# Kernel tuning notes

Measured on AMD Instinct MI355X. Metric: run time of the kernel, lower is better.

## Reference

```python
import jax, jax.numpy as jnp
import numpy as np

HIDDEN = 256
HEADS = 8
HEAD_DIM = HIDDEN // HEADS
SCALE = HEAD_DIM ** -0.5
N = 4096
NUM_GRAPHS = 16
LN_EPS = 1e-5


def setup_inputs() -> dict:
    key = jax.random.key(0)
    ks = jax.random.split(key, 8)
    x = jax.random.normal(ks[0], (N, HIDDEN), dtype=jnp.float32)
    batch = jnp.sort(jax.random.randint(ks[1], (N,), 0, NUM_GRAPHS, dtype=jnp.int64))
    # Xavier-uniform linear weights, stored as [in, out] (y = x @ W + b)
    lim = float(np.sqrt(6.0 / (HIDDEN + HIDDEN)))
    def W(k):
        return jax.random.uniform(k, (HIDDEN, HIDDEN), jnp.float32, -lim, lim)
    return {
        "x": x,
        "batch": batch,
        "Wq": W(ks[2]), "bq": jnp.zeros((HIDDEN,), jnp.float32),
        "Wk": W(ks[3]), "bk": jnp.zeros((HIDDEN,), jnp.float32),
        "Wv": W(ks[4]), "bv": jnp.zeros((HIDDEN,), jnp.float32),
        "Wo": W(ks[5]), "bo": jnp.zeros((HIDDEN,), jnp.float32),
        "gamma": jnp.ones((HIDDEN,), jnp.float32),
        "beta": jnp.zeros((HIDDEN,), jnp.float32),
    }


def _layer_norm(x, gamma, beta):
    mu = jnp.mean(x, axis=-1, keepdims=True)
    var = jnp.mean(jnp.square(x - mu), axis=-1, keepdims=True)
    return (x - mu) * jax.lax.rsqrt(var + LN_EPS) * gamma + beta


def reference(x, batch, Wq, bq, Wk, bk, Wv, bv, Wo, bo, gamma, beta):
    residual = x
    h = _layer_norm(x, gamma, beta)
    n = h.shape[0]
    q = (h @ Wq + bq).reshape(n, HEADS, HEAD_DIM)
    k = (h @ Wk + bk).reshape(n, HEADS, HEAD_DIM)
    v = (h @ Wv + bv).reshape(n, HEADS, HEAD_DIM)
    # dense scores masked to block-diagonal (same-graph) structure
    scores = jnp.einsum('ihd,jhd->ihj', q, k) * SCALE  # [N, H, N]
    same_graph = (batch[None, :] == batch[:, None])[:, None, :]  # [N, 1, N]
    scores = jnp.where(same_graph, scores, -jnp.inf)
    attn = jax.nn.softmax(scores, axis=-1)
    attn = jnp.nan_to_num(attn, nan=0.0)
    out = jnp.einsum('ihj,jhd->ihd', attn, v).reshape(n, HIDDEN)
    out = out @ Wo + bo
    return residual + out
```

## Files before the change

kernel.cpp:

```cpp
#include <hip/hip_runtime.h>

#define NNODES 4096
#define HID 256
#define NG 16
#define NH 8
#define HD 32
#define LN_EPS 1e-5f
#define QSCALE (0.17677669529663687f * 1.4426950408889634f)
#define CAPT 384
#define KLS 40
#define VTS (CAPT + 2)

typedef unsigned short u16;
typedef unsigned int u32;
typedef __bf16 bf16x8 __attribute__((ext_vector_type(8)));
typedef float f32x4 __attribute__((ext_vector_type(4)));

__device__ __forceinline__ float bf2f(u16 u){
  union { u32 i; float f; } c; c.i = ((u32)u) << 16; return c.f;
}
__device__ __forceinline__ u16 f2bf(float f){
  union { float f; u32 i; } c; c.f = f;
  u32 x = c.i;
  return (u16)((x + 0x7fffu + ((x >> 16) & 1u)) >> 16);
}

__global__ __launch_bounds__(256) void prep_kernel(
    const float* __restrict__ x, const float* __restrict__ gamma,
    const float* __restrict__ beta, u16* __restrict__ h,
    const float* __restrict__ Wq, const float* __restrict__ Wk,
    const float* __restrict__ Wv, const float* __restrict__ Wo,
    u16* __restrict__ Wt, const int* __restrict__ bw, int* __restrict__ seg){
  __shared__ u16 tile[32][33];
  __shared__ int bad;
  int b = blockIdx.x;
  if (b < 1024){
    int wave = threadIdx.x >> 6, lane = threadIdx.x & 63;
    int row = b * 4 + wave;
    float4 xv = ((const float4*)x)[row * 64 + lane];
    float a0 = xv.x, a1 = xv.y, a2 = xv.z, a3 = xv.w;
    float s = a0 + a1 + a2 + a3;
    #pragma unroll
    for (int m = 1; m < 64; m <<= 1) s += __shfl_xor(s, m);
    float mu = s * (1.0f / HID);
    float d0 = a0 - mu, d1 = a1 - mu, d2 = a2 - mu, d3 = a3 - mu;
    float vv = d0*d0 + d1*d1 + d2*d2 + d3*d3;
    #pragma unroll
    for (int m = 1; m < 64; m <<= 1) vv += __shfl_xor(vv, m);
    float rs = rsqrtf(vv * (1.0f / HID) + LN_EPS);
    float4 gv = ((const float4*)gamma)[lane];
    float4 bv = ((const float4*)beta)[lane];
    ushort4 o;
    o.x = f2bf(d0 * rs * gv.x + bv.x);
    o.y = f2bf(d1 * rs * gv.y + bv.y);
    o.z = f2bf(d2 * rs * gv.z + bv.z);
    o.w = f2bf(d3 * rs * gv.w + bv.w);
    *(ushort4*)(h + (size_t)row * HID + lane * 4) = o;
  } else if (b < 1280){
    int idx = b - 1024;
    int w = idx >> 6;
    int t = idx & 63;
    int bx = (t & 7) * 32, by = (t >> 3) * 32;
    const float* src = (w == 0) ? Wq : (w == 1) ? Wk : (w == 2) ? Wv : Wo;
    u16* dst = Wt + (size_t)w * HID * HID;
    int tx = threadIdx.x & 31, ty = threadIdx.x >> 5;
    #pragma unroll
    for (int r = 0; r < 32; r += 8)
      tile[ty + r][tx] = f2bf(src[(size_t)(by + ty + r) * HID + bx + tx]);
    __syncthreads();
    #pragma unroll
    for (int r = 0; r < 32; r += 8)
      dst[(size_t)(bx + ty + r) * HID + by + tx] = tile[tx][ty + r];
  } else {
    if (threadIdx.x == 0) bad = 0;
    __syncthreads();
    int local_bad = 0;
    for (int i = threadIdx.x; i < NNODES; i += 256){
      int v = bw[i];
      if (v < 0 || v > 15) local_bad = 1;
      if (i + 1 < NNODES && bw[i + 1] < v) local_bad = 1;
    }
    if (local_bad) atomicOr(&bad, 1);
    __syncthreads();
    int stride = bad ? 2 : 1;
    int g = threadIdx.x;
    if (g <= NG){
      int lo = 0, hi = NNODES;
      while (lo < hi){
        int mid = (lo + hi) >> 1;
        if (bw[mid * stride] < g) lo = mid + 1; else hi = mid;
      }
      seg[g] = lo;
    }
  }
}

template<bool FINAL>
__device__ __forceinline__ void gemm_tile(const u16* __restrict__ A, const u16* __restrict__ Bt,
    const float* __restrict__ bias, const float* __restrict__ resid, void* __restrict__ out){
  int gw = blockIdx.x * 4 + (threadIdx.x >> 6);
  int lane = threadIdx.x & 63;
  int lr = lane & 15, lq = lane >> 4;
  int m0 = (gw >> 4) * 64;
  int n0 = (gw & 15) * 16;
  f32x4 acc[4] = {};
  const u16* arow = A + (size_t)(m0 + lr) * HID + lq * 8;
  const u16* brow = Bt + (size_t)(n0 + lr) * HID + lq * 8;
  #pragma unroll
  for (int k0 = 0; k0 < HID; k0 += 32){
    bf16x8 b = *(const bf16x8*)(brow + k0);
    #pragma unroll
    for (int t = 0; t < 4; t++){
      bf16x8 a = *(const bf16x8*)(arow + (size_t)t * 16 * HID + k0);
      acc[t] = __builtin_amdgcn_mfma_f32_16x16x32_bf16(a, b, acc[t], 0, 0, 0);
    }
  }
  int col = n0 + lr;
  float bb = bias[col];
  #pragma unroll
  for (int t = 0; t < 4; t++){
    #pragma unroll
    for (int r = 0; r < 4; r++){
      int row = m0 + 16 * t + lq * 4 + r;
      float val = acc[t][r] + bb;
      if (FINAL){
        val += resid[(size_t)row * HID + col];
        ((float*)out)[(size_t)row * HID + col] = val;
      } else {
        ((u16*)out)[(size_t)row * HID + col] = f2bf(val);
      }
    }
  }
}

__global__ __launch_bounds__(256) void gemm_qkv_kernel(const u16* __restrict__ h,
    const u16* __restrict__ Wt, const float* __restrict__ bq, const float* __restrict__ bk,
    const float* __restrict__ bv, u16* __restrict__ q, u16* __restrict__ k, u16* __restrict__ v){
  int which = blockIdx.y;
  const u16* B = Wt + (size_t)which * HID * HID;
  const float* bias = (which == 0) ? bq : (which == 1) ? bk : bv;
  u16* out = (which == 0) ? q : (which == 1) ? k : v;
  gemm_tile<false>(h, B, bias, nullptr, out);
}

__global__ __launch_bounds__(256) void gemm_proj_kernel(const u16* __restrict__ ao,
    const u16* __restrict__ WtO, const float* __restrict__ bo, const float* __restrict__ x,
    float* __restrict__ out){
  gemm_tile<true>(ao, WtO, bo, x, out);
}

__global__ __launch_bounds__(512, 4) void attn_kernel(const u16* __restrict__ q,
    const u16* __restrict__ k, const u16* __restrict__ v, const int* __restrict__ seg,
    u16* __restrict__ out){
  __shared__ u16 kl[CAPT * KLS];
  __shared__ u16 vt[HD * VTS];
  __shared__ float mg[4][10][64];
  int gh = blockIdx.y;
  int g = gh >> 3, hd = gh & 7;
  int start = seg[g], end = seg[g + 1];
  int len = end - start;
  if (len <= 0) return;
  if (len > CAPT) len = CAPT;
  int ntj = (len + 15) >> 4;
  int nj16 = ntj << 4;
  for (int idx = threadIdx.x; idx < nj16 * 4; idx += 512){
    int row = idx >> 2, part = idx & 3;
    uint4 val = make_uint4(0, 0, 0, 0);
    if (row < len)
      val = *(const uint4*)&k[(size_t)(start + row) * HID + hd * HD + part * 8];
    *(uint4*)&kl[row * KLS + part * 8] = val;
  }
  for (int idx = threadIdx.x; idx < nj16 * 4; idx += 512){
    int row = idx >> 2, part = idx & 3;
    uint4 w = make_uint4(0, 0, 0, 0);
    if (row < len)
      w = *(const uint4*)&v[(size_t)(start + row) * HID + hd * HD + part * 8];
    int d0 = part * 8;
    vt[(d0 + 0) * VTS + row] = (u16)(w.x & 0xffffu);
    vt[(d0 + 1) * VTS + row] = (u16)(w.x >> 16);
    vt[(d0 + 2) * VTS + row] = (u16)(w.y & 0xffffu);
    vt[(d0 + 3) * VTS + row] = (u16)(w.y >> 16);
    vt[(d0 + 4) * VTS + row] = (u16)(w.z & 0xffffu);
    vt[(d0 + 5) * VTS + row] = (u16)(w.z >> 16);
    vt[(d0 + 6) * VTS + row] = (u16)(w.w & 0xffffu);
    vt[(d0 + 7) * VTS + row] = (u16)(w.w >> 16);
  }
  __syncthreads();
  int wave = threadIdx.x >> 6, lane = threadIdx.x & 63;
  int lq = lane >> 4, lr = lane & 15;
  int tl = wave & 3;
  int jh = wave >> 2;
  int nouter = (ntj + 15) >> 4;
  for (int it = 0; it < nouter; it++){
    int tq = it * 16 + blockIdx.x * 4 + tl;
    bool active = tq < ntj;
    int q0 = tq << 4;
    float m = -3.0e38f, l = 0.f;
    f32x4 o0 = {0.f,0.f,0.f,0.f}, o1 = {0.f,0.f,0.f,0.f};
    if (active){
      bf16x8 qf = *(const bf16x8*)&q[(size_t)(start + q0 + lr) * HID + hd * HD + lq * 8];
      int half = (ntj + 1) >> 1;
      int jt0 = jh ? half : 0;
      int jt1 = jh ? ntj : half;
      for (int jt = jt0; jt < jt1; jt++){
        int j0 = jt << 4;
        bf16x8 kf = *(const bf16x8*)&kl[(j0 + lr) * KLS + lq * 8];
        f32x4 st = __builtin_amdgcn_mfma_f32_16x16x32_bf16(kf, qf,
                     (f32x4){0.f,0.f,0.f,0.f}, 0, 0, 0);
        int jb = j0 + lq * 4;
        float s0 = (jb + 0 < len) ? st[0] * QSCALE : -3.0e38f;
        float s1 = (jb + 1 < len) ? st[1] * QSCALE : -3.0e38f;
        float s2 = (jb + 2 < len) ? st[2] * QSCALE : -3.0e38f;
        float s3 = (jb + 3 < len) ? st[3] * QSCALE : -3.0e38f;
        float tm = fmaxf(fmaxf(s0, s1), fmaxf(s2, s3));
        tm = fmaxf(tm, __shfl_xor(tm, 16));
        tm = fmaxf(tm, __shfl_xor(tm, 32));
        float mn = fmaxf(m, tm);
        float alpha = exp2f(m - mn);
        float p0 = exp2f(s0 - mn), p1 = exp2f(s1 - mn);
        float p2 = exp2f(s2 - mn), p3 = exp2f(s3 - mn);
        float ps = (p0 + p1) + (p2 + p3);
        ps += __shfl_xor(ps, 16);
        ps += __shfl_xor(ps, 32);
        l = l * alpha + ps;
        m = mn;
        union { bf16x8 v8; u32 w[4]; } pf, vf0, vf1;
        pf.w[0] = (u32)f2bf(p0) | ((u32)f2bf(p1) << 16);
        pf.w[1] = (u32)f2bf(p2) | ((u32)f2bf(p3) << 16);
        pf.w[2] = 0; pf.w[3] = 0;
        const u16* vp0 = &vt[lr * VTS + j0 + lq * 4];
        const u16* vp1 = &vt[(16 + lr) * VTS + j0 + lq * 4];
        vf0.w[0] = *(const u32*)vp0; vf0.w[1] = *(const u32*)(vp0 + 2);
        vf0.w[2] = 0; vf0.w[3] = 0;
        vf1.w[0] = *(const u32*)vp1; vf1.w[1] = *(const u32*)(vp1 + 2);
        vf1.w[2] = 0; vf1.w[3] = 0;
        o0 = o0 * alpha;
        o1 = o1 * alpha;
        o0 = __builtin_amdgcn_mfma_f32_16x16x32_bf16(vf0.v8, pf.v8, o0, 0, 0, 0);
        o1 = __builtin_amdgcn_mfma_f32_16x16x32_bf16(vf1.v8, pf.v8, o1, 0, 0, 0);
      }
    }
    if (jh == 1){
      mg[tl][0][lane] = o0[0]; mg[tl][1][lane] = o0[1];
      mg[tl][2][lane] = o0[2]; mg[tl][3][lane] = o0[3];
      mg[tl][4][lane] = o1[0]; mg[tl][5][lane] = o1[1];
      mg[tl][6][lane] = o1[2]; mg[tl][7][lane] = o1[3];
      mg[tl][8][lane] = m;     mg[tl][9][lane] = l;
    }
    __syncthreads();
    if (jh == 0 && active && q0 + lr < len){
      float m2 = mg[tl][8][lane], l2 = mg[tl][9][lane];
      float mn = fmaxf(m, m2);
      float a  = exp2f(m - mn);
      float a2 = exp2f(m2 - mn);
      float lt = l * a + l2 * a2;
      float rl = 1.0f / lt;
      float r0 = (o0[0]*a + mg[tl][0][lane]*a2) * rl;
      float r1 = (o0[1]*a + mg[tl][1][lane]*a2) * rl;
      float r2 = (o0[2]*a + mg[tl][2][lane]*a2) * rl;
      float r3 = (o0[3]*a + mg[tl][3][lane]*a2) * rl;
      float r4 = (o1[0]*a + mg[tl][4][lane]*a2) * rl;
      float r5 = (o1[1]*a + mg[tl][5][lane]*a2) * rl;
      float r6 = (o1[2]*a + mg[tl][6][lane]*a2) * rl;
      float r7 = (o1[3]*a + mg[tl][7][lane]*a2) * rl;
      u16* orow = out + (size_t)(start + q0 + lr) * HID + hd * HD;
      int dbase = lq * 4;
      *(u32*)&orow[dbase]          = (u32)f2bf(r0) | ((u32)f2bf(r1) << 16);
      *(u32*)&orow[dbase + 2]      = (u32)f2bf(r2) | ((u32)f2bf(r3) << 16);
      *(u32*)&orow[16 + dbase]     = (u32)f2bf(r4) | ((u32)f2bf(r5) << 16);
      *(u32*)&orow[16 + dbase + 2] = (u32)f2bf(r6) | ((u32)f2bf(r7) << 16);
    }
    __syncthreads();
  }
}

__global__ void sentinel_kernel(u32* __restrict__ out, int nwords){
  int i = blockIdx.x * 256 + threadIdx.x;
  if (i < nwords) out[i] = 0x46404640u;
}

extern "C" void kernel_launch(void* const* d_in, const int* in_sizes, int n_in,
                              void* d_out, int out_size, void* d_ws, size_t ws_size,
                              hipStream_t stream){
  const float* x   = (const float*)d_in[0];
  const int* batch = (const int*)d_in[1];
  const float* Wq = (const float*)d_in[2],  *bq = (const float*)d_in[3];
  const float* Wk = (const float*)d_in[4],  *bk = (const float*)d_in[5];
  const float* Wv = (const float*)d_in[6],  *bv = (const float*)d_in[7];
  const float* Wo = (const float*)d_in[8],  *bo = (const float*)d_in[9];
  const float* gamma = (const float*)d_in[10], *beta = (const float*)d_in[11];

  const size_t WT_OFF  = 1024;
  const size_t QKV_OFF = WT_OFF + 4 * HID * HID * 2;
  const size_t BUF     = (size_t)NNODES * HID * 2;
  const size_t NEED    = QKV_OFF + 4 * BUF;

  if (ws_size < NEED){
    int nwords = out_size / 2;
    sentinel_kernel<<<(nwords + 255) / 256, 256, 0, stream>>>((u32*)d_out, nwords);
    return;
  }

  char* w = (char*)d_ws;
  int* seg  = (int*)(w + 128);
  u16* Wt   = (u16*)(w + WT_OFF);
  u16* qb   = (u16*)(w + QKV_OFF);
  u16* kb   = qb + (size_t)NNODES * HID;
  u16* vb   = kb + (size_t)NNODES * HID;
  u16* ao   = vb + (size_t)NNODES * HID;
  u16* h    = (u16*)d_out;

  prep_kernel<<<1281, 256, 0, stream>>>(x, gamma, beta, h, Wq, Wk, Wv, Wo, Wt, batch, seg);
  gemm_qkv_kernel<<<dim3(256, 3), 256, 0, stream>>>(h, Wt, bq, bk, bv, qb, kb, vb);
  attn_kernel<<<dim3(4, NG * NH), 512, 0, stream>>>(qb, kb, vb, seg, ao);
  gemm_proj_kernel<<<256, 256, 0, stream>>>(ao, Wt + 3 * (size_t)HID * HID, bo, x, (float*)d_out);
}
```

Measured before the change: 128.7 us.

## Fuse QKV projection into attention kernel per graph-head block

Removes the separate QKV GEMM kernel and computes K and V for the whole graph segment and Q for the block's query tiles directly inside the attention kernel, writing them to shared memory instead of global buffers. Each of the two blocks per (graph, head) redundantly recomputes the full K/V projection for its segment. The split-key two-wave merge with its extra shared buffer and barriers is dropped: each wave now processes all key tiles for its query tile. This saves a kernel launch and the global round-trip for q/k/v. In exchange it duplicates K/V compute across blocks and reads weights straight from global/L2 without tiling reuse.

```diff
diff --git a/kernel.cpp b/kernel.cpp
--- a/kernel.cpp
+++ b/kernel.cpp
@@ -10,6 +10,7 @@
 #define CAPT 384
 #define KLS 40
 #define VTS (CAPT + 2)
+#define QSL 12
 
 typedef unsigned short u16;
 typedef unsigned int u32;
@@ -133,144 +134,144 @@
   }
 }
 
-__global__ __launch_bounds__(256) void gemm_qkv_kernel(const u16* __restrict__ h,
-    const u16* __restrict__ Wt, const float* __restrict__ bq, const float* __restrict__ bk,
-    const float* __restrict__ bv, u16* __restrict__ q, u16* __restrict__ k, u16* __restrict__ v){
-  int which = blockIdx.y;
-  const u16* B = Wt + (size_t)which * HID * HID;
-  const float* bias = (which == 0) ? bq : (which == 1) ? bk : bv;
-  u16* out = (which == 0) ? q : (which == 1) ? k : v;
-  gemm_tile<false>(h, B, bias, nullptr, out);
-}
-
 __global__ __launch_bounds__(256) void gemm_proj_kernel(const u16* __restrict__ ao,
     const u16* __restrict__ WtO, const float* __restrict__ bo, const float* __restrict__ x,
     float* __restrict__ out){
   gemm_tile<true>(ao, WtO, bo, x, out);
 }
 
-__global__ __launch_bounds__(512, 4) void attn_kernel(const u16* __restrict__ q,
-    const u16* __restrict__ k, const u16* __restrict__ v, const int* __restrict__ seg,
+__global__ __launch_bounds__(512, 4) void qkv_attn_kernel(
+    const u16* __restrict__ h, const u16* __restrict__ Wt,
+    const float* __restrict__ bq, const float* __restrict__ bk,
+    const float* __restrict__ bv, const int* __restrict__ seg,
     u16* __restrict__ out){
   __shared__ u16 kl[CAPT * KLS];
   __shared__ u16 vt[HD * VTS];
-  __shared__ float mg[4][10][64];
+  __shared__ u16 ql[QSL * 16 * KLS];
   int gh = blockIdx.y;
   int g = gh >> 3, hd = gh & 7;
+  int bid = blockIdx.x;
   int start = seg[g], end = seg[g + 1];
   int len = end - start;
   if (len <= 0) return;
   if (len > CAPT) len = CAPT;
   int ntj = (len + 15) >> 4;
-  int nj16 = ntj << 4;
-  for (int idx = threadIdx.x; idx < nj16 * 4; idx += 512){
-    int row = idx >> 2, part = idx & 3;
-    uint4 val = make_uint4(0, 0, 0, 0);
-    if (row < len)
-      val = *(const uint4*)&k[(size_t)(start + row) * HID + hd * HD + part * 8];
-    *(uint4*)&kl[row * KLS + part * 8] = val;
-  }
-  for (int idx = threadIdx.x; idx < nj16 * 4; idx += 512){
-    int row = idx >> 2, part = idx & 3;
-    uint4 w = make_uint4(0, 0, 0, 0);
-    if (row < len)
-      w = *(const uint4*)&v[(size_t)(start + row) * HID + hd * HD + part * 8];
-    int d0 = part * 8;
-    vt[(d0 + 0) * VTS + row] = (u16)(w.x & 0xffffu);
-    vt[(d0 + 1) * VTS + row] = (u16)(w.x >> 16);
-    vt[(d0 + 2) * VTS + row] = (u16)(w.y & 0xffffu);
-    vt[(d0 + 3) * VTS + row] = (u16)(w.y >> 16);
-    vt[(d0 + 4) * VTS + row] = (u16)(w.z & 0xffffu);
-    vt[(d0 + 5) * VTS + row] = (u16)(w.z >> 16);
-    vt[(d0 + 6) * VTS + row] = (u16)(w.w & 0xffffu);
-    vt[(d0 + 7) * VTS + row] = (u16)(w.w >> 16);
-  }
-  __syncthreads();
   int wave = threadIdx.x >> 6, lane = threadIdx.x & 63;
   int lq = lane >> 4, lr = lane & 15;
-  int tl = wave & 3;
-  int jh = wave >> 2;
-  int nouter = (ntj + 15) >> 4;
-  for (int it = 0; it < nouter; it++){
-    int tq = it * 16 + blockIdx.x * 4 + tl;
-    bool active = tq < ntj;
-    int q0 = tq << 4;
+
+  const u16* wq0p = Wt + (size_t)(hd * HD + lr) * HID;
+  const u16* wk0p = wq0p + (size_t)HID * HID;
+  const u16* wv0p = wq0p + (size_t)2 * HID * HID;
+  float bq0 = bq[hd * HD + lr],      bq1 = bq[hd * HD + 16 + lr];
+  float bk0 = bk[hd * HD + lr],      bk1 = bk[hd * HD + 16 + lr];
+  float bv0 = bv[hd * HD + lr],      bv1 = bv[hd * HD + 16 + lr];
+
+  for (int t = wave; t < ntj; t += 8){
+    f32x4 ak0 = {}, ak1 = {}, av0 = {}, av1 = {};
+    int row = start + (t << 4) + lr;
+    if (row >= NNODES) row = NNODES - 1;
+    const u16* hrow = h + (size_t)row * HID + lq * 8;
+    #pragma unroll 2
+    for (int k0 = 0; k0 < HID; k0 += 32){
+      bf16x8 a    = *(const bf16x8*)(hrow + k0);
+      bf16x8 wk0f = *(const bf16x8*)(wk0p + k0 + lq * 8);
+      bf16x8 wk1f = *(const bf16x8*)(wk0p + 16 * HID + k0 + lq * 8);
+      bf16x8 wv0f = *(const bf16x8*)(wv0p + k0 + lq * 8);
+      bf16x8 wv1f = *(const bf16x8*)(wv0p + 16 * HID + k0 + lq * 8);
+      ak0 = __builtin_amdgcn_mfma_f32_16x16x32_bf16(a, wk0f, ak0, 0, 0, 0);
+      ak1 = __builtin_amdgcn_mfma_f32_16x16x32_bf16(a, wk1f, ak1, 0, 0, 0);
+      av0 = __builtin_amdgcn_mfma_f32_16x16x32_bf16(a, wv0f, av0, 0, 0, 0);
+      av1 = __builtin_amdgcn_mfma_f32_16x16x32_bf16(a, wv1f, av1, 0, 0, 0);
+    }
+    int jr = (t << 4) + lq * 4;
+    #pragma unroll
+    for (int r = 0; r < 4; r++){
+      kl[(jr + r) * KLS + lr]      = f2bf(ak0[r] + bk0);
+      kl[(jr + r) * KLS + 16 + lr] = f2bf(ak1[r] + bk1);
+    }
+    *(u32*)&vt[lr * VTS + jr]            = (u32)f2bf(av0[0] + bv0) | ((u32)f2bf(av0[1] + bv0) << 16);
+    *(u32*)&vt[lr * VTS + jr + 2]        = (u32)f2bf(av0[2] + bv0) | ((u32)f2bf(av0[3] + bv0) << 16);
+    *(u32*)&vt[(16 + lr) * VTS + jr]     = (u32)f2bf(av1[0] + bv1) | ((u32)f2bf(av1[1] + bv1) << 16);
+    *(u32*)&vt[(16 + lr) * VTS + jr + 2] = (u32)f2bf(av1[2] + bv1) | ((u32)f2bf(av1[3] + bv1) << 16);
+  }
+
+  for (int s = wave; s < QSL; s += 8){
+    int t = (s << 1) + bid;
+    if (t >= ntj) continue;
+    f32x4 aq0 = {}, aq1 = {};
+    int row = start + (t << 4) + lr;
+    if (row >= NNODES) row = NNODES - 1;
+    const u16* hrow = h + (size_t)row * HID + lq * 8;
+    #pragma unroll 2
+    for (int k0 = 0; k0 < HID; k0 += 32){
+      bf16x8 a    = *(const bf16x8*)(hrow + k0);
+      bf16x8 wq0f = *(const bf16x8*)(wq0p + k0 + lq * 8);
+      bf16x8 wq1f = *(const bf16x8*)(wq0p + 16 * HID + k0 + lq * 8);
+      aq0 = __builtin_amdgcn_mfma_f32_16x16x32_bf16(a, wq0f, aq0, 0, 0, 0);
+      aq1 = __builtin_amdgcn_mfma_f32_16x16x32_bf16(a, wq1f, aq1, 0, 0, 0);
+    }
+    int qr = (s << 4) + lq * 4;
+    #pragma unroll
+    for (int r = 0; r < 4; r++){
+      ql[(qr + r) * KLS + lr]      = f2bf(aq0[r] + bq0);
+      ql[(qr + r) * KLS + 16 + lr] = f2bf(aq1[r] + bq1);
+    }
+  }
+  __syncthreads();
+
+  for (int s = wave; s < QSL; s += 8){
+    int t = (s << 1) + bid;
+    if (t >= ntj) continue;
+    int q0 = t << 4;
+    bf16x8 qf = *(const bf16x8*)&ql[((s << 4) + lr) * KLS + lq * 8];
     float m = -3.0e38f, l = 0.f;
     f32x4 o0 = {0.f,0.f,0.f,0.f}, o1 = {0.f,0.f,0.f,0.f};
-    if (active){
-      bf16x8 qf = *(const bf16x8*)&q[(size_t)(start + q0 + lr) * HID + hd * HD + lq * 8];
-      int half = (ntj + 1) >> 1;
-      int jt0 = jh ? half : 0;
-      int jt1 = jh ? ntj : half;
-      for (int jt = jt0; jt < jt1; jt++){
-        int j0 = jt << 4;
-        bf16x8 kf = *(const bf16x8*)&kl[(j0 + lr) * KLS + lq * 8];
-        f32x4 st = __builtin_amdgcn_mfma_f32_16x16x32_bf16(kf, qf,
-                     (f32x4){0.f,0.f,0.f,0.f}, 0, 0, 0);
-        int jb = j0 + lq * 4;
-        float s0 = (jb + 0 < len) ? st[0] * QSCALE : -3.0e38f;
-        float s1 = (jb + 1 < len) ? st[1] * QSCALE : -3.0e38f;
-        float s2 = (jb + 2 < len) ? st[2] * QSCALE : -3.0e38f;
-        float s3 = (jb + 3 < len) ? st[3] * QSCALE : -3.0e38f;
-        float tm = fmaxf(fmaxf(s0, s1), fmaxf(s2, s3));
-        tm = fmaxf(tm, __shfl_xor(tm, 16));
-        tm = fmaxf(tm, __shfl_xor(tm, 32));
-        float mn = fmaxf(m, tm);
-        float alpha = exp2f(m - mn);
-        float p0 = exp2f(s0 - mn), p1 = exp2f(s1 - mn);
-        float p2 = exp2f(s2 - mn), p3 = exp2f(s3 - mn);
-        float ps = (p0 + p1) + (p2 + p3);
-        ps += __shfl_xor(ps, 16);
-        ps += __shfl_xor(ps, 32);
-        l = l * alpha + ps;
-        m = mn;
-        union { bf16x8 v8; u32 w[4]; } pf, vf0, vf1;
-        pf.w[0] = (u32)f2bf(p0) | ((u32)f2bf(p1) << 16);
-        pf.w[1] = (u32)f2bf(p2) | ((u32)f2bf(p3) << 16);
-        pf.w[2] = 0; pf.w[3] = 0;
-        const u16* vp0 = &vt[lr * VTS + j0 + lq * 4];
-        const u16* vp1 = &vt[(16 + lr) * VTS + j0 + lq * 4];
-        vf0.w[0] = *(const u32*)vp0; vf0.w[1] = *(const u32*)(vp0 + 2);
-        vf0.w[2] = 0; vf0.w[3] = 0;
-        vf1.w[0] = *(const u32*)vp1; vf1.w[1] = *(const u32*)(vp1 + 2);
-        vf1.w[2] = 0; vf1.w[3] = 0;
-        o0 = o0 * alpha;
-        o1 = o1 * alpha;
-        o0 = __builtin_amdgcn_mfma_f32_16x16x32_bf16(vf0.v8, pf.v8, o0, 0, 0, 0);
-        o1 = __builtin_amdgcn_mfma_f32_16x16x32_bf16(vf1.v8, pf.v8, o1, 0, 0, 0);
-      }
-    }
-    if (jh == 1){
-      mg[tl][0][lane] = o0[0]; mg[tl][1][lane] = o0[1];
-      mg[tl][2][lane] = o0[2]; mg[tl][3][lane] = o0[3];
-      mg[tl][4][lane] = o1[0]; mg[tl][5][lane] = o1[1];
-      mg[tl][6][lane] = o1[2]; mg[tl][7][lane] = o1[3];
-      mg[tl][8][lane] = m;     mg[tl][9][lane] = l;
-    }
-    __syncthreads();
-    if (jh == 0 && active && q0 + lr < len){
-      float m2 = mg[tl][8][lane], l2 = mg[tl][9][lane];
-      float mn = fmaxf(m, m2);
-      float a  = exp2f(m - mn);
-      float a2 = exp2f(m2 - mn);
-      float lt = l * a + l2 * a2;
-      float rl = 1.0f / lt;
-      float r0 = (o0[0]*a + mg[tl][0][lane]*a2) * rl;
-      float r1 = (o0[1]*a + mg[tl][1][lane]*a2) * rl;
-      float r2 = (o0[2]*a + mg[tl][2][lane]*a2) * rl;
-      float r3 = (o0[3]*a + mg[tl][3][lane]*a2) * rl;
-      float r4 = (o1[0]*a + mg[tl][4][lane]*a2) * rl;
-      float r5 = (o1[1]*a + mg[tl][5][lane]*a2) * rl;
-      float r6 = (o1[2]*a + mg[tl][6][lane]*a2) * rl;
-      float r7 = (o1[3]*a + mg[tl][7][lane]*a2) * rl;
+    for (int jt = 0; jt < ntj; jt++){
+      int j0 = jt << 4;
+      bf16x8 kf = *(const bf16x8*)&kl[(j0 + lr) * KLS + lq * 8];
+      f32x4 st = __builtin_amdgcn_mfma_f32_16x16x32_bf16(kf, qf,
+                   (f32x4){0.f,0.f,0.f,0.f}, 0, 0, 0);
+      int jb = j0 + lq * 4;
+      float s0 = (jb + 0 < len) ? st[0] * QSCALE : -3.0e38f;
+      float s1 = (jb + 1 < len) ? st[1] * QSCALE : -3.0e38f;
+      float s2 = (jb + 2 < len) ? st[2] * QSCALE : -3.0e38f;
+      float s3 = (jb + 3 < len) ? st[3] * QSCALE : -3.0e38f;
+      float tm = fmaxf(fmaxf(s0, s1), fmaxf(s2, s3));
+      tm = fmaxf(tm, __shfl_xor(tm, 16));
+      tm = fmaxf(tm, __shfl_xor(tm, 32));
+      float mn = fmaxf(m, tm);
+      float alpha = exp2f(m - mn);
+      float p0 = exp2f(s0 - mn), p1 = exp2f(s1 - mn);
+      float p2 = exp2f(s2 - mn), p3 = exp2f(s3 - mn);
+      float ps = (p0 + p1) + (p2 + p3);
+      ps += __shfl_xor(ps, 16);
+      ps += __shfl_xor(ps, 32);
+      l = l * alpha + ps;
+      m = mn;
+      union { bf16x8 v8; u32 w[4]; } pf, vf0, vf1;
+      pf.w[0] = (u32)f2bf(p0) | ((u32)f2bf(p1) << 16);
+      pf.w[1] = (u32)f2bf(p2) | ((u32)f2bf(p3) << 16);
+      pf.w[2] = 0; pf.w[3] = 0;
+      const u16* vp0 = &vt[lr * VTS + j0 + lq * 4];
+      const u16* vp1 = &vt[(16 + lr) * VTS + j0 + lq * 4];
+      vf0.w[0] = *(const u32*)vp0; vf0.w[1] = *(const u32*)(vp0 + 2);
+      vf0.w[2] = 0; vf0.w[3] = 0;
+      vf1.w[0] = *(const u32*)vp1; vf1.w[1] = *(const u32*)(vp1 + 2);
+      vf1.w[2] = 0; vf1.w[3] = 0;
+      o0 = o0 * alpha;
+      o1 = o1 * alpha;
+      o0 = __builtin_amdgcn_mfma_f32_16x16x32_bf16(vf0.v8, pf.v8, o0, 0, 0, 0);
+      o1 = __builtin_amdgcn_mfma_f32_16x16x32_bf16(vf1.v8, pf.v8, o1, 0, 0, 0);
+    }
+    if (q0 + lr < len){
+      float rl = 1.0f / l;
       u16* orow = out + (size_t)(start + q0 + lr) * HID + hd * HD;
       int dbase = lq * 4;
-      *(u32*)&orow[dbase]          = (u32)f2bf(r0) | ((u32)f2bf(r1) << 16);
-      *(u32*)&orow[dbase + 2]      = (u32)f2bf(r2) | ((u32)f2bf(r3) << 16);
-      *(u32*)&orow[16 + dbase]     = (u32)f2bf(r4) | ((u32)f2bf(r5) << 16);
-      *(u32*)&orow[16 + dbase + 2] = (u32)f2bf(r6) | ((u32)f2bf(r7) << 16);
-    }
-    __syncthreads();
+      *(u32*)&orow[dbase]          = (u32)f2bf(o0[0]*rl) | ((u32)f2bf(o0[1]*rl) << 16);
+      *(u32*)&orow[dbase + 2]      = (u32)f2bf(o0[2]*rl) | ((u32)f2bf(o0[3]*rl) << 16);
+      *(u32*)&orow[16 + dbase]     = (u32)f2bf(o1[0]*rl) | ((u32)f2bf(o1[1]*rl) << 16);
+      *(u32*)&orow[16 + dbase + 2] = (u32)f2bf(o1[2]*rl) | ((u32)f2bf(o1[3]*rl) << 16);
+    }
   }
 }
 
@@ -290,10 +291,10 @@
   const float* Wo = (const float*)d_in[8],  *bo = (const float*)d_in[9];
   const float* gamma = (const float*)d_in[10], *beta = (const float*)d_in[11];
 
-  const size_t WT_OFF  = 1024;
-  const size_t QKV_OFF = WT_OFF + 4 * HID * HID * 2;
-  const size_t BUF     = (size_t)NNODES * HID * 2;
-  const size_t NEED    = QKV_OFF + 4 * BUF;
+  const size_t WT_OFF = 1024;
+  const size_t AO_OFF = WT_OFF + 4 * HID * HID * 2;
+  const size_t BUF    = (size_t)NNODES * HID * 2;
+  const size_t NEED   = AO_OFF + BUF;
 
   if (ws_size < NEED){
     int nwords = out_size / 2;
@@ -304,14 +305,10 @@
   char* w = (char*)d_ws;
   int* seg  = (int*)(w + 128);
   u16* Wt   = (u16*)(w + WT_OFF);
-  u16* qb   = (u16*)(w + QKV_OFF);
-  u16* kb   = qb + (size_t)NNODES * HID;
-  u16* vb   = kb + (size_t)NNODES * HID;
-  u16* ao   = vb + (size_t)NNODES * HID;
+  u16* ao   = (u16*)(w + AO_OFF);
   u16* h    = (u16*)d_out;
 
   prep_kernel<<<1281, 256, 0, stream>>>(x, gamma, beta, h, Wq, Wk, Wv, Wo, Wt, batch, seg);
-  gemm_qkv_kernel<<<dim3(256, 3), 256, 0, stream>>>(h, Wt, bq, bk, bv, qb, kb, vb);
-  attn_kernel<<<dim3(4, NG * NH), 512, 0, stream>>>(qb, kb, vb, seg, ao);
+  qkv_attn_kernel<<<dim3(2, NG * NH), 512, 0, stream>>>(h, Wt, bq, bk, bv, seg, ao);
   gemm_proj_kernel<<<256, 256, 0, stream>>>(ao, Wt + 3 * (size_t)HID * HID, bo, x, (float*)d_out);
 }
```

Result: slower. 136.0 us (+5.7%).

## Fuse all stages into one cooperative persistent kernel with grid syncs

Applied to the files above, without the earlier changes.

Replaces the four separate launches (prep, QKV GEMM, attention, output projection) with a single cooperative kernel of 512 blocks that runs each phase in turn, separated by grid-wide barriers. It falls back to four ordinary launches if the cooperative launch fails. The QKV GEMM now computes Q, K and V together in each wave so the A tile is loaded once. Attention drops the split of key tiles across two wave halves and the shared-memory merge, so each wave processes all key tiles for its query tile. The aim is to remove launch gaps and tail effects between kernels, at the cost of grid-sync overhead, fewer blocks resident per stage, and less parallelism inside attention.

```diff
diff --git a/kernel.cpp b/kernel.cpp
--- a/kernel.cpp
+++ b/kernel.cpp
@@ -1,4 +1,7 @@
 #include <hip/hip_runtime.h>
+#include <hip/hip_cooperative_groups.h>
+
+namespace cg = cooperative_groups;
 
 #define NNODES 4096
 #define HID 256
@@ -16,28 +19,33 @@
 typedef __bf16 bf16x8 __attribute__((ext_vector_type(8)));
 typedef float f32x4 __attribute__((ext_vector_type(4)));
 
-__device__ __forceinline__ float bf2f(u16 u){
-  union { u32 i; float f; } c; c.i = ((u32)u) << 16; return c.f;
-}
 __device__ __forceinline__ u16 f2bf(float f){
   union { float f; u32 i; } c; c.f = f;
   u32 x = c.i;
   return (u16)((x + 0x7fffu + ((x >> 16) & 1u)) >> 16);
 }
 
-__global__ __launch_bounds__(256) void prep_kernel(
-    const float* __restrict__ x, const float* __restrict__ gamma,
-    const float* __restrict__ beta, u16* __restrict__ h,
-    const float* __restrict__ Wq, const float* __restrict__ Wk,
-    const float* __restrict__ Wv, const float* __restrict__ Wo,
-    u16* __restrict__ Wt, const int* __restrict__ bw, int* __restrict__ seg){
+struct Params {
+  const float* x; const int* batch;
+  const float* Wq; const float* bq;
+  const float* Wk; const float* bk;
+  const float* Wv; const float* bv;
+  const float* Wo; const float* bo;
+  const float* gamma; const float* beta;
+  int* seg; u16* Wt; u16* h; u16* qb; u16* kb; u16* vb; u16* ao;
+  float* out;
+};
+
+__device__ __forceinline__ void phaseA(const Params& p){
   __shared__ u16 tile[32][33];
   __shared__ int bad;
-  int b = blockIdx.x;
-  if (b < 1024){
-    int wave = threadIdx.x >> 6, lane = threadIdx.x & 63;
-    int row = b * 4 + wave;
-    float4 xv = ((const float4*)x)[row * 64 + lane];
+  int bid = blockIdx.x, tid = threadIdx.x;
+  int wave = tid >> 6, lane = tid & 63;
+  int wgid = bid * 4 + wave;
+  #pragma unroll
+  for (int ps = 0; ps < 2; ps++){
+    int row = wgid + ps * 2048;
+    float4 xv = ((const float4*)p.x)[row * 64 + lane];
     float a0 = xv.x, a1 = xv.y, a2 = xv.z, a3 = xv.w;
     float s = a0 + a1 + a2 + a3;
     #pragma unroll
@@ -48,22 +56,22 @@
     #pragma unroll
     for (int m = 1; m < 64; m <<= 1) vv += __shfl_xor(vv, m);
     float rs = rsqrtf(vv * (1.0f / HID) + LN_EPS);
-    float4 gv = ((const float4*)gamma)[lane];
-    float4 bv = ((const float4*)beta)[lane];
+    float4 gv = ((const float4*)p.gamma)[lane];
+    float4 bv = ((const float4*)p.beta)[lane];
     ushort4 o;
     o.x = f2bf(d0 * rs * gv.x + bv.x);
     o.y = f2bf(d1 * rs * gv.y + bv.y);
     o.z = f2bf(d2 * rs * gv.z + bv.z);
     o.w = f2bf(d3 * rs * gv.w + bv.w);
-    *(ushort4*)(h + (size_t)row * HID + lane * 4) = o;
-  } else if (b < 1280){
-    int idx = b - 1024;
-    int w = idx >> 6;
-    int t = idx & 63;
+    *(ushort4*)(p.h + (size_t)row * HID + lane * 4) = o;
+  }
+  if (bid < 256){
+    int w = bid >> 6;
+    int t = bid & 63;
     int bx = (t & 7) * 32, by = (t >> 3) * 32;
-    const float* src = (w == 0) ? Wq : (w == 1) ? Wk : (w == 2) ? Wv : Wo;
-    u16* dst = Wt + (size_t)w * HID * HID;
-    int tx = threadIdx.x & 31, ty = threadIdx.x >> 5;
+    const float* src = (w == 0) ? p.Wq : (w == 1) ? p.Wk : (w == 2) ? p.Wv : p.Wo;
+    u16* dst = p.Wt + (size_t)w * HID * HID;
+    int tx = tid & 31, ty = tid >> 5;
     #pragma unroll
     for (int r = 0; r < 32; r += 8)
       tile[ty + r][tx] = f2bf(src[(size_t)(by + ty + r) * HID + bx + tx]);
@@ -71,11 +79,13 @@
     #pragma unroll
     for (int r = 0; r < 32; r += 8)
       dst[(size_t)(bx + ty + r) * HID + by + tx] = tile[tx][ty + r];
-  } else {
-    if (threadIdx.x == 0) bad = 0;
+  }
+  if (bid == 511){
+    const int* bw = p.batch;
+    if (tid == 0) bad = 0;
     __syncthreads();
     int local_bad = 0;
-    for (int i = threadIdx.x; i < NNODES; i += 256){
+    for (int i = tid; i < NNODES; i += 256){
       int v = bw[i];
       if (v < 0 || v > 15) local_bad = 1;
       if (i + 1 < NNODES && bw[i + 1] < v) local_bad = 1;
@@ -83,98 +93,82 @@
     if (local_bad) atomicOr(&bad, 1);
     __syncthreads();
     int stride = bad ? 2 : 1;
-    int g = threadIdx.x;
+    int g = tid;
     if (g <= NG){
       int lo = 0, hi = NNODES;
       while (lo < hi){
         int mid = (lo + hi) >> 1;
         if (bw[mid * stride] < g) lo = mid + 1; else hi = mid;
       }
-      seg[g] = lo;
-    }
-  }
-}
-
-template<bool FINAL>
-__device__ __forceinline__ void gemm_tile(const u16* __restrict__ A, const u16* __restrict__ Bt,
-    const float* __restrict__ bias, const float* __restrict__ resid, void* __restrict__ out){
-  int gw = blockIdx.x * 4 + (threadIdx.x >> 6);
+      p.seg[g] = lo;
+    }
+  }
+}
+
+__device__ __forceinline__ void phaseB(const Params& p){
+  int wgid = blockIdx.x * 4 + (threadIdx.x >> 6);
   int lane = threadIdx.x & 63;
   int lr = lane & 15, lq = lane >> 4;
-  int m0 = (gw >> 4) * 64;
-  int n0 = (gw & 15) * 16;
-  f32x4 acc[4] = {};
-  const u16* arow = A + (size_t)(m0 + lr) * HID + lq * 8;
-  const u16* brow = Bt + (size_t)(n0 + lr) * HID + lq * 8;
+  int m0 = (wgid >> 4) * 32, n0 = (wgid & 15) * 16;
+  const u16* a0p = p.h + (size_t)(m0 + lr) * HID + lq * 8;
+  const u16* a1p = a0p + (size_t)16 * HID;
+  const u16* bqp = p.Wt + (size_t)(n0 + lr) * HID + lq * 8;
+  const u16* bkp = bqp + (size_t)HID * HID;
+  const u16* bvp = bqp + (size_t)2 * HID * HID;
+  f32x4 aq[2] = {}, ak[2] = {}, av[2] = {};
   #pragma unroll
   for (int k0 = 0; k0 < HID; k0 += 32){
-    bf16x8 b = *(const bf16x8*)(brow + k0);
-    #pragma unroll
-    for (int t = 0; t < 4; t++){
-      bf16x8 a = *(const bf16x8*)(arow + (size_t)t * 16 * HID + k0);
-      acc[t] = __builtin_amdgcn_mfma_f32_16x16x32_bf16(a, b, acc[t], 0, 0, 0);
-    }
+    bf16x8 a0 = *(const bf16x8*)(a0p + k0);
+    bf16x8 a1 = *(const bf16x8*)(a1p + k0);
+    bf16x8 wq = *(const bf16x8*)(bqp + k0);
+    bf16x8 wk = *(const bf16x8*)(bkp + k0);
+    bf16x8 wv = *(const bf16x8*)(bvp + k0);
+    aq[0] = __builtin_amdgcn_mfma_f32_16x16x32_bf16(a0, wq, aq[0], 0, 0, 0);
+    aq[1] = __builtin_amdgcn_mfma_f32_16x16x32_bf16(a1, wq, aq[1], 0, 0, 0);
+    ak[0] = __builtin_amdgcn_mfma_f32_16x16x32_bf16(a0, wk, ak[0], 0, 0, 0);
+    ak[1] = __builtin_amdgcn_mfma_f32_16x16x32_bf16(a1, wk, ak[1], 0, 0, 0);
+    av[0] = __builtin_amdgcn_mfma_f32_16x16x32_bf16(a0, wv, av[0], 0, 0, 0);
+    av[1] = __builtin_amdgcn_mfma_f32_16x16x32_bf16(a1, wv, av[1], 0, 0, 0);
   }
   int col = n0 + lr;
-  float bb = bias[col];
-  #pragma unroll
-  for (int t = 0; t < 4; t++){
+  float cq = p.bq[col], ck = p.bk[col], cv = p.bv[col];
+  #pragma unroll
+  for (int t = 0; t < 2; t++){
     #pragma unroll
     for (int r = 0; r < 4; r++){
-      int row = m0 + 16 * t + lq * 4 + r;
-      float val = acc[t][r] + bb;
-      if (FINAL){
-        val += resid[(size_t)row * HID + col];
-        ((float*)out)[(size_t)row * HID + col] = val;
-      } else {
-        ((u16*)out)[(size_t)row * HID + col] = f2bf(val);
-      }
-    }
-  }
-}
-
-__global__ __launch_bounds__(256) void gemm_qkv_kernel(const u16* __restrict__ h,
-    const u16* __restrict__ Wt, const float* __restrict__ bq, const float* __restrict__ bk,
-    const float* __restrict__ bv, u16* __restrict__ q, u16* __restrict__ k, u16* __restrict__ v){
-  int which = blockIdx.y;
-  const u16* B = Wt + (size_t)which * HID * HID;
-  const float* bias = (which == 0) ? bq : (which == 1) ? bk : bv;
-  u16* out = (which == 0) ? q : (which == 1) ? k : v;
-  gemm_tile<false>(h, B, bias, nullptr, out);
-}
-
-__global__ __launch_bounds__(256) void gemm_proj_kernel(const u16* __restrict__ ao,
-    const u16* __restrict__ WtO, const float* __restrict__ bo, const float* __restrict__ x,
-    float* __restrict__ out){
-  gemm_tile<true>(ao, WtO, bo, x, out);
-}
-
-__global__ __launch_bounds__(512, 4) void attn_kernel(const u16* __restrict__ q,
-    const u16* __restrict__ k, const u16* __restrict__ v, const int* __restrict__ seg,
-    u16* __restrict__ out){
+      size_t row = (size_t)(m0 + 16 * t + lq * 4 + r) * HID + col;
+      p.qb[row] = f2bf(aq[t][r] + cq);
+      p.kb[row] = f2bf(ak[t][r] + ck);
+      p.vb[row] = f2bf(av[t][r] + cv);
+    }
+  }
+}
+
+__device__ __forceinline__ void phaseC(const Params& p){
   __shared__ u16 kl[CAPT * KLS];
   __shared__ u16 vt[HD * VTS];
-  __shared__ float mg[4][10][64];
-  int gh = blockIdx.y;
+  int job = blockIdx.x;
+  int quarter = job & 3, gh = job >> 2;
   int g = gh >> 3, hd = gh & 7;
-  int start = seg[g], end = seg[g + 1];
+  int start = p.seg[g], end = p.seg[g + 1];
   int len = end - start;
   if (len <= 0) return;
   if (len > CAPT) len = CAPT;
   int ntj = (len + 15) >> 4;
   int nj16 = ntj << 4;
-  for (int idx = threadIdx.x; idx < nj16 * 4; idx += 512){
+  int tid = threadIdx.x;
+  for (int idx = tid; idx < nj16 * 4; idx += 256){
     int row = idx >> 2, part = idx & 3;
     uint4 val = make_uint4(0, 0, 0, 0);
     if (row < len)
-      val = *(const uint4*)&k[(size_t)(start + row) * HID + hd * HD + part * 8];
+      val = *(const uint4*)&p.kb[(size_t)(start + row) * HID + hd * HD + part * 8];
     *(uint4*)&kl[row * KLS + part * 8] = val;
   }
-  for (int idx = threadIdx.x; idx < nj16 * 4; idx += 512){
+  for (int idx = tid; idx < nj16 * 4; idx += 256){
     int row = idx >> 2, part = idx & 3;
     uint4 w = make_uint4(0, 0, 0, 0);
     if (row < len)
-      w = *(const uint4*)&v[(size_t)(start + row) * HID + hd * HD + part * 8];
+      w = *(const uint4*)&p.vb[(size_t)(start + row) * HID + hd * HD + part * 8];
     int d0 = part * 8;
     vt[(d0 + 0) * VTS + row] = (u16)(w.x & 0xffffu);
     vt[(d0 + 1) * VTS + row] = (u16)(w.x >> 16);
@@ -186,93 +180,111 @@
     vt[(d0 + 7) * VTS + row] = (u16)(w.w >> 16);
   }
   __syncthreads();
-  int wave = threadIdx.x >> 6, lane = threadIdx.x & 63;
+  int wave = tid >> 6, lane = tid & 63;
   int lq = lane >> 4, lr = lane & 15;
-  int tl = wave & 3;
-  int jh = wave >> 2;
   int nouter = (ntj + 15) >> 4;
   for (int it = 0; it < nouter; it++){
-    int tq = it * 16 + blockIdx.x * 4 + tl;
-    bool active = tq < ntj;
+    int tq = it * 16 + quarter * 4 + wave;
+    if (tq >= ntj) continue;
     int q0 = tq << 4;
+    bf16x8 qf = *(const bf16x8*)&p.qb[(size_t)(start + q0 + lr) * HID + hd * HD + lq * 8];
     float m = -3.0e38f, l = 0.f;
     f32x4 o0 = {0.f,0.f,0.f,0.f}, o1 = {0.f,0.f,0.f,0.f};
-    if (active){
-      bf16x8 qf = *(const bf16x8*)&q[(size_t)(start + q0 + lr) * HID + hd * HD + lq * 8];
-      int half = (ntj + 1) >> 1;
-      int jt0 = jh ? half : 0;
-      int jt1 = jh ? ntj : half;
-      for (int jt = jt0; jt < jt1; jt++){
-        int j0 = jt << 4;
-        bf16x8 kf = *(const bf16x8*)&kl[(j0 + lr) * KLS + lq * 8];
-        f32x4 st = __builtin_amdgcn_mfma_f32_16x16x32_bf16(kf, qf,
-                     (f32x4){0.f,0.f,0.f,0.f}, 0, 0, 0);
-        int jb = j0 + lq * 4;
-        float s0 = (jb + 0 < len) ? st[0] * QSCALE : -3.0e38f;
-        float s1 = (jb + 1 < len) ? st[1] * QSCALE : -3.0e38f;
-        float s2 = (jb + 2 < len) ? st[2] * QSCALE : -3.0e38f;
-        float s3 = (jb + 3 < len) ? st[3] * QSCALE : -3.0e38f;
-        float tm = fmaxf(fmaxf(s0, s1), fmaxf(s2, s3));
-        tm = fmaxf(tm, __shfl_xor(tm, 16));
-        tm = fmaxf(tm, __shfl_xor(tm, 32));
-        float mn = fmaxf(m, tm);
-        float alpha = exp2f(m - mn);
-        float p0 = exp2f(s0 - mn), p1 = exp2f(s1 - mn);
-        float p2 = exp2f(s2 - mn), p3 = exp2f(s3 - mn);
-        float ps = (p0 + p1) + (p2 + p3);
-        ps += __shfl_xor(ps, 16);
-        ps += __shfl_xor(ps, 32);
-        l = l * alpha + ps;
-        m = mn;
-        union { bf16x8 v8; u32 w[4]; } pf, vf0, vf1;
-        pf.w[0] = (u32)f2bf(p0) | ((u32)f2bf(p1) << 16);
-        pf.w[1] = (u32)f2bf(p2) | ((u32)f2bf(p3) << 16);
-        pf.w[2] = 0; pf.w[3] = 0;
-        const u16* vp0 = &vt[lr * VTS + j0 + lq * 4];
-        const u16* vp1 = &vt[(16 + lr) * VTS + j0 + lq * 4];
-        vf0.w[0] = *(const u32*)vp0; vf0.w[1] = *(const u32*)(vp0 + 2);
-        vf0.w[2] = 0; vf0.w[3] = 0;
-        vf1.w[0] = *(const u32*)vp1; vf1.w[1] = *(const u32*)(vp1 + 2);
-        vf1.w[2] = 0; vf1.w[3] = 0;
-        o0 = o0 * alpha;
-        o1 = o1 * alpha;
-        o0 = __builtin_amdgcn_mfma_f32_16x16x32_bf16(vf0.v8, pf.v8, o0, 0, 0, 0);
-        o1 = __builtin_amdgcn_mfma_f32_16x16x32_bf16(vf1.v8, pf.v8, o1, 0, 0, 0);
-      }
-    }
-    if (jh == 1){
-      mg[tl][0][lane] = o0[0]; mg[tl][1][lane] = o0[1];
-      mg[tl][2][lane] = o0[2]; mg[tl][3][lane] = o0[3];
-      mg[tl][4][lane] = o1[0]; mg[tl][5][lane] = o1[1];
-      mg[tl][6][lane] = o1[2]; mg[tl][7][lane] = o1[3];
-      mg[tl][8][lane] = m;     mg[tl][9][lane] = l;
-    }
-    __syncthreads();
-    if (jh == 0 && active && q0 + lr < len){
-      float m2 = mg[tl][8][lane], l2 = mg[tl][9][lane];
-      float mn = fmaxf(m, m2);
-      float a  = exp2f(m - mn);
-      float a2 = exp2f(m2 - mn);
-      float lt = l * a + l2 * a2;
-      float rl = 1.0f / lt;
-      float r0 = (o0[0]*a + mg[tl][0][lane]*a2) * rl;
-      float r1 = (o0[1]*a + mg[tl][1][lane]*a2) * rl;
-      float r2 = (o0[2]*a + mg[tl][2][lane]*a2) * rl;
-      float r3 = (o0[3]*a + mg[tl][3][lane]*a2) * rl;
-      float r4 = (o1[0]*a + mg[tl][4][lane]*a2) * rl;
-      float r5 = (o1[1]*a + mg[tl][5][lane]*a2) * rl;
-      float r6 = (o1[2]*a + mg[tl][6][lane]*a2) * rl;
-      float r7 = (o1[3]*a + mg[tl][7][lane]*a2) * rl;
-      u16* orow = out + (size_t)(start + q0 + lr) * HID + hd * HD;
+    for (int jt = 0; jt < ntj; jt++){
+      int j0 = jt << 4;
+      bf16x8 kf = *(const bf16x8*)&kl[(j0 + lr) * KLS + lq * 8];
+      f32x4 st = __builtin_amdgcn_mfma_f32_16x16x32_bf16(kf, qf,
+                   (f32x4){0.f,0.f,0.f,0.f}, 0, 0, 0);
+      int jb = j0 + lq * 4;
+      float s0 = (jb + 0 < len) ? st[0] * QSCALE : -3.0e38f;
+      float s1 = (jb + 1 < len) ? st[1] * QSCALE : -3.0e38f;
+      float s2 = (jb + 2 < len) ? st[2] * QSCALE : -3.0e38f;
+      float s3 = (jb + 3 < len) ? st[3] * QSCALE : -3.0e38f;
+      float tm = fmaxf(fmaxf(s0, s1), fmaxf(s2, s3));
+      tm = fmaxf(tm, __shfl_xor(tm, 16));
+      tm = fmaxf(tm, __shfl_xor(tm, 32));
+      float mn = fmaxf(m, tm);
+      float alpha = exp2f(m - mn);
+      float p0 = exp2f(s0 - mn), p1 = exp2f(s1 - mn);
+      float p2 = exp2f(s2 - mn), p3 = exp2f(s3 - mn);
+      float ps = (p0 + p1) + (p2 + p3);
+      ps += __shfl_xor(ps, 16);
+      ps += __shfl_xor(ps, 32);
+      l = l * alpha + ps;
+      m = mn;
+      union { bf16x8 v8; u32 w[4]; } pf, vf0, vf1;
+      pf.w[0] = (u32)f2bf(p0) | ((u32)f2bf(p1) << 16);
+      pf.w[1] = (u32)f2bf(p2) | ((u32)f2bf(p3) << 16);
+      pf.w[2] = 0; pf.w[3] = 0;
+      const u16* vp0 = &vt[lr * VTS + j0 + lq * 4];
+      const u16* vp1 = &vt[(16 + lr) * VTS + j0 + lq * 4];
+      vf0.w[0] = *(const u32*)vp0; vf0.w[1] = *(const u32*)(vp0 + 2);
+      vf0.w[2] = 0; vf0.w[3] = 0;
+      vf1.w[0] = *(const u32*)vp1; vf1.w[1] = *(const u32*)(vp1 + 2);
+      vf1.w[2] = 0; vf1.w[3] = 0;
+      o0 = o0 * alpha;
+      o1 = o1 * alpha;
+      o0 = __builtin_amdgcn_mfma_f32_16x16x32_bf16(vf0.v8, pf.v8, o0, 0, 0, 0);
+      o1 = __builtin_amdgcn_mfma_f32_16x16x32_bf16(vf1.v8, pf.v8, o1, 0, 0, 0);
+    }
+    if (q0 + lr < len){
+      float rl = 1.0f / l;
+      u16* orow = p.ao + (size_t)(start + q0 + lr) * HID + hd * HD;
       int dbase = lq * 4;
-      *(u32*)&orow[dbase]          = (u32)f2bf(r0) | ((u32)f2bf(r1) << 16);
-      *(u32*)&orow[dbase + 2]      = (u32)f2bf(r2) | ((u32)f2bf(r3) << 16);
-      *(u32*)&orow[16 + dbase]     = (u32)f2bf(r4) | ((u32)f2bf(r5) << 16);
-      *(u32*)&orow[16 + dbase + 2] = (u32)f2bf(r6) | ((u32)f2bf(r7) << 16);
-    }
-    __syncthreads();
-  }
-}
+      *(u32*)&orow[dbase]          = (u32)f2bf(o0[0]*rl) | ((u32)f2bf(o0[1]*rl) << 16);
+      *(u32*)&orow[dbase + 2]      = (u32)f2bf(o0[2]*rl) | ((u32)f2bf(o0[3]*rl) << 16);
+      *(u32*)&orow[16 + dbase]     = (u32)f2bf(o1[0]*rl) | ((u32)f2bf(o1[1]*rl) << 16);
+      *(u32*)&orow[16 + dbase + 2] = (u32)f2bf(o1[2]*rl) | ((u32)f2bf(o1[3]*rl) << 16);
+    }
+  }
+}
+
+__device__ __forceinline__ void phaseD(const Params& p){
+  int wgid = blockIdx.x * 4 + (threadIdx.x >> 6);
+  int lane = threadIdx.x & 63;
+  int lr = lane & 15, lq = lane >> 4;
+  int m0 = (wgid >> 4) * 32, n0 = (wgid & 15) * 16;
+  const u16* a0p = p.ao + (size_t)(m0 + lr) * HID + lq * 8;
+  const u16* a1p = a0p + (size_t)16 * HID;
+  const u16* bp  = p.Wt + (size_t)3 * HID * HID + (size_t)(n0 + lr) * HID + lq * 8;
+  f32x4 acc[2] = {};
+  #pragma unroll
+  for (int k0 = 0; k0 < HID; k0 += 32){
+    bf16x8 b  = *(const bf16x8*)(bp + k0);
+    bf16x8 a0 = *(const bf16x8*)(a0p + k0);
+    bf16x8 a1 = *(const bf16x8*)(a1p + k0);
+    acc[0] = __builtin_amdgcn_mfma_f32_16x16x32_bf16(a0, b, acc[0], 0, 0, 0);
+    acc[1] = __builtin_amdgcn_mfma_f32_16x16x32_bf16(a1, b, acc[1], 0, 0, 0);
+  }
+  int col = n0 + lr;
+  float bb = p.bo[col];
+  #pragma unroll
+  for (int t = 0; t < 2; t++){
+    #pragma unroll
+    for (int r = 0; r < 4; r++){
+      size_t row = (size_t)(m0 + 16 * t + lq * 4 + r) * HID + col;
+      p.out[row] = acc[t][r] + bb + p.x[row];
+    }
+  }
+}
+
+__global__ __launch_bounds__(256, 2) void fused_kernel(Params p){
+  phaseA(p);
+  __threadfence();
+  cg::this_grid().sync();
+  phaseB(p);
+  __threadfence();
+  cg::this_grid().sync();
+  phaseC(p);
+  __threadfence();
+  cg::this_grid().sync();
+  phaseD(p);
+}
+
+__global__ __launch_bounds__(256, 2) void kA(Params p){ phaseA(p); }
+__global__ __launch_bounds__(256, 2) void kB(Params p){ phaseB(p); }
+__global__ __launch_bounds__(256, 2) void kC(Params p){ phaseC(p); }
+__global__ __launch_bounds__(256, 2) void kD(Params p){ phaseD(p); }
 
 __global__ void sentinel_kernel(u32* __restrict__ out, int nwords){
   int i = blockIdx.x * 256 + threadIdx.x;
@@ -282,18 +294,10 @@
 extern "C" void kernel_launch(void* const* d_in, const int* in_sizes, int n_in,
                               void* d_out, int out_size, void* d_ws, size_t ws_size,
                               hipStream_t stream){
-  const float* x   = (const float*)d_in[0];
-  const int* batch = (const int*)d_in[1];
-  const float* Wq = (const float*)d_in[2],  *bq = (const float*)d_in[3];
-  const float* Wk = (const float*)d_in[4],  *bk = (const float*)d_in[5];
-  const float* Wv = (const float*)d_in[6],  *bv = (const float*)d_in[7];
-  const float* Wo = (const float*)d_in[8],  *bo = (const float*)d_in[9];
-  const float* gamma = (const float*)d_in[10], *beta = (const float*)d_in[11];
-
-  const size_t WT_OFF  = 1024;
-  const size_t QKV_OFF = WT_OFF + 4 * HID * HID * 2;
-  const size_t BUF     = (size_t)NNODES * HID * 2;
-  const size_t NEED    = QKV_OFF + 4 * BUF;
+  const size_t WT_OFF = 1024;
+  const size_t H_OFF  = WT_OFF + 4 * HID * HID * 2;
+  const size_t BUF    = (size_t)NNODES * HID * 2;
+  const size_t NEED   = H_OFF + 5 * BUF;
 
   if (ws_size < NEED){
     int nwords = out_size / 2;
@@ -302,16 +306,30 @@
   }
 
   char* w = (char*)d_ws;
-  int* seg  = (int*)(w + 128);
-  u16* Wt   = (u16*)(w + WT_OFF);
-  u16* qb   = (u16*)(w + QKV_OFF);
-  u16* kb   = qb + (size_t)NNODES * HID;
-  u16* vb   = kb + (size_t)NNODES * HID;
-  u16* ao   = vb + (size_t)NNODES * HID;
-  u16* h    = (u16*)d_out;
-
-  prep_kernel<<<1281, 256, 0, stream>>>(x, gamma, beta, h, Wq, Wk, Wv, Wo, Wt, batch, seg);
-  gemm_qkv_kernel<<<dim3(256, 3), 256, 0, stream>>>(h, Wt, bq, bk, bv, qb, kb, vb);
-  attn_kernel<<<dim3(4, NG * NH), 512, 0, stream>>>(qb, kb, vb, seg, ao);
-  gemm_proj_kernel<<<256, 256, 0, stream>>>(ao, Wt + 3 * (size_t)HID * HID, bo, x, (float*)d_out);
-}
+  Params prm;
+  prm.x     = (const float*)d_in[0];
+  prm.batch = (const int*)d_in[1];
+  prm.Wq = (const float*)d_in[2];  prm.bq = (const float*)d_in[3];
+  prm.Wk = (const float*)d_in[4];  prm.bk = (const float*)d_in[5];
+  prm.Wv = (const float*)d_in[6];  prm.bv = (const float*)d_in[7];
+  prm.Wo = (const float*)d_in[8];  prm.bo = (const float*)d_in[9];
+  prm.gamma = (const float*)d_in[10]; prm.beta = (const float*)d_in[11];
+  prm.seg = (int*)(w + 128);
+  prm.Wt  = (u16*)(w + WT_OFF);
+  prm.h   = (u16*)(w + H_OFF);
+  prm.qb  = prm.h  + (size_t)NNODES * HID;
+  prm.kb  = prm.qb + (size_t)NNODES * HID;
+  prm.vb  = prm.kb + (size_t)NNODES * HID;
+  prm.ao  = prm.vb + (size_t)NNODES * HID;
+  prm.out = (float*)d_out;
+
+  void* args[] = { (void*)&prm };
+  hipError_t e = hipLaunchCooperativeKernel((const void*)fused_kernel,
+                                            dim3(512), dim3(256), args, 0, stream);
+  if (e != hipSuccess){
+    kA<<<512, 256, 0, stream>>>(prm);
+    kB<<<512, 256, 0, stream>>>(prm);
+    kC<<<512, 256, 0, stream>>>(prm);
+    kD<<<512, 256, 0, stream>>>(prm);
+  }
+}
```

New measurement: 466.1 us. 3.62x slower.
